# Kernel optimization log

Hardware: AMD Instinct MI355X
Metric: run time of the kernel (lower is better)

## Reference

```python
import jax, jax.numpy as jnp
import numpy as np

N_NODES = 50000
N_EDGES = 800000
D = 128


def gcn_conv(x, edge_index, W, b):
    """PyG GCNConv: out = D^{-1/2} (A+I) D^{-1/2} (x W) + b."""
    n = x.shape[0]
    loop = jnp.arange(n)
    row = jnp.concatenate([edge_index[0], loop])  # source nodes (x_j)
    col = jnp.concatenate([edge_index[1], loop])  # target nodes (aggregation)
    deg = jnp.zeros((n,), dtype=x.dtype).at[col].add(1.0)
    deg_inv_sqrt = jnp.where(deg > 0, jax.lax.rsqrt(deg), 0.0)
    norm = deg_inv_sqrt[row] * deg_inv_sqrt[col]  # [E+N]
    h = x @ W  # [N, F]
    msg = h[row] * norm[:, None]  # gather + scale, [E+N, F]
    out = jax.ops.segment_sum(msg, col, num_segments=n)
    return out + b


def setup_inputs() -> dict:
    key = jax.random.key(0)
    k1, k2, k3, k4 = jax.random.split(key, 4)
    x = jax.random.normal(k1, (N_NODES, D), dtype=jnp.float32)
    edge_index = jax.random.randint(k2, (2, N_EDGES), 0, N_NODES, dtype=jnp.int64)
    scale = 1.0 / np.sqrt(D)
    W1 = jax.random.normal(k3, (D, D), dtype=jnp.float32) * scale
    W2 = jax.random.normal(k4, (D, D), dtype=jnp.float32) * scale
    b1 = jnp.zeros((D,), dtype=jnp.float32)
    b2 = jnp.zeros((D,), dtype=jnp.float32)
    return {"x": x, "edge_index": edge_index, "W1": W1, "b1": b1, "W2": W2, "b2": b2}


def reference(x, edge_index, W1, b1, W2, b2):
    h = gcn_conv(x, edge_index, W1, b1)
    h = gcn_conv(h, edge_index, W2, b2)
    return jax.nn.leaky_relu(h, negative_slope=0.1)
```

## Files before the change

### kernel.cpp

```cpp
#include <hip/hip_runtime.h>

#define DF 128
#define CHUNK 2048
#define LSTCAP 6144

typedef __bf16 bf16x8 __attribute__((ext_vector_type(8)));
typedef float f32x4 __attribute__((ext_vector_type(4)));


static __device__ __forceinline__ float lrelu(float x) {
  return x > 0.f ? x : 0.1f * x;
}
static __device__ __forceinline__ unsigned short f2bf(float f) {
  unsigned int u = __float_as_uint(f);
  u += 0x7FFFu + ((u >> 16) & 1u);
  return (unsigned short)(u >> 16);
}
static __device__ __forceinline__ float bf2f(unsigned short h) {
  return __uint_as_float((unsigned int)h << 16);
}

__global__ __launch_bounds__(256) void prep_kernel(
    const float* __restrict__ W1, const float* __restrict__ W2,
    const float* __restrict__ b1, unsigned short* __restrict__ wfrag,
    float* __restrict__ c1, const void* __restrict__ ei, int E,
    int* __restrict__ M, unsigned int* __restrict__ pairs, int NBUCK,
    int NCHUNK) {
  __shared__ int h[256];
  __shared__ int any32;
  int tid = threadIdx.x;
  if (blockIdx.x < 129) {
    if (tid >= 128) return;
    int j = tid;
    if (blockIdx.x < 128) {
      int i = blockIdx.x;
      float acc = 0.f;
      for (int k = 0; k < 128; ++k)
        acc = fmaf(W1[i * 128 + k], W2[k * 128 + j], acc);
      unsigned short hh = f2bf(acc);
      unsigned short ll = f2bf(acc - bf2f(hh));
      int fid = (((i >> 5) * 8) + (j >> 4)) * 64 + ((i >> 3) & 3) * 16 + (j & 15);
      int pos = fid * 8 + (i & 7);
      wfrag[pos] = hh;
      wfrag[16384 + pos] = ll;
    } else {
      float acc = 0.f;
      for (int k = 0; k < 128; ++k) acc = fmaf(b1[k], W2[k * 128 + j], acc);
      c1[j] = acc;
    }
    return;
  }
  int blk = blockIdx.x - 129;
  if (tid == 0) any32 = 0;
  h[tid] = 0;
  __syncthreads();
  int base = blk * CHUNK;
  int end = min(base + CHUNK, E);
  {
    const unsigned int* u = (const unsigned int*)ei;
    long long i = (long long)base + tid * 8;
    if (i < end && u[2 * i + 1] != 0u) any32 = 1;
  }
  __syncthreads();
  int is64 = !any32;
  if (is64) {
    const long long* p = (const long long*)ei;
    for (int i = base + tid; i < end; i += 256) {
      int src = (int)p[i];
      int c = (int)p[(size_t)E + i];
      atomicAdd(&h[c >> 8], 1);
      pairs[i] = ((unsigned)src << 16) | (unsigned)c;
    }
  } else {
    const int* p = (const int*)ei;
    for (int i = base + tid; i < end; i += 256) {
      int src = p[i];
      int c = p[(size_t)E + i];
      atomicAdd(&h[c >> 8], 1);
      pairs[i] = ((unsigned)src << 16) | (unsigned)c;
    }
  }
  __syncthreads();
  if (tid < NBUCK) M[tid * NCHUNK + blk] = h[tid];
}

__global__ __launch_bounds__(256) void matscanA_kernel(int* __restrict__ M,
                                                       int* __restrict__ btot,
                                                       int NCHUNK) {
  __shared__ int s[256];
  int tid = threadIdx.x;
  int base = blockIdx.x * NCHUNK;
  int i0 = tid * 2, i1 = tid * 2 + 1;
  int v0 = (i0 < NCHUNK) ? M[base + i0] : 0;
  int v1 = (i1 < NCHUNK) ? M[base + i1] : 0;
  int loc = v0 + v1;
  s[tid] = loc;
  __syncthreads();
  for (int d = 1; d < 256; d <<= 1) {
    int add = (tid >= d) ? s[tid - d] : 0;
    __syncthreads();
    s[tid] += add;
    __syncthreads();
  }
  int excl = s[tid] - loc;
  if (i0 < NCHUNK) M[base + i0] = excl;
  if (i1 < NCHUNK) M[base + i1] = excl + v0;
  if (tid == 255) btot[blockIdx.x] = s[255];
}

__global__ __launch_bounds__(256) void p1c_kernel(
    const unsigned int* __restrict__ pairs, int E, const int* __restrict__ M,
    const int* __restrict__ btot, int NBUCK, int NCHUNK,
    unsigned int* __restrict__ staging) {
  __shared__ int bs[256];
  __shared__ int rowM[256];
  __shared__ int lcur[256];
  int tid = threadIdx.x;
  int blk = blockIdx.x;
  int v = (tid < NBUCK) ? btot[tid] : 0;
  bs[tid] = v;
  __syncthreads();
  for (int d = 1; d < 256; d <<= 1) {
    int add = (tid >= d) ? bs[tid - d] : 0;
    __syncthreads();
    bs[tid] += add;
    __syncthreads();
  }
  if (tid < NBUCK) rowM[tid] = M[tid * NCHUNK + blk] + (bs[tid] - v);
  lcur[tid] = 0;
  __syncthreads();
  int base = blk * CHUNK;
  int end = min(base + CHUNK, E);
  for (int i = base + tid; i < end; i += 256) {
    unsigned pv = pairs[i];
    int b = (int)((pv & 0xFFFFu) >> 8);
    int r = atomicAdd(&lcur[b], 1);
    staging[rowM[b] + r] = pv;
  }
}

__global__ __launch_bounds__(256) void p2_kernel(
    const unsigned int* __restrict__ staging, const int* __restrict__ btot,
    int NBUCK, int2* __restrict__ offcnt, float* __restrict__ dis,
    unsigned short* __restrict__ srcs, int n) {
  __shared__ int bs[256], h[256], ex[256], lcur[256];
  __shared__ unsigned int lst[LSTCAP];
  int tid = threadIdx.x;
  int b = blockIdx.x;
  int v = (tid < NBUCK) ? btot[tid] : 0;
  bs[tid] = v;
  h[tid] = 0;
  lcur[tid] = 0;
  __syncthreads();
  for (int d = 1; d < 256; d <<= 1) {
    int add = (tid >= d) ? bs[tid - d] : 0;
    __syncthreads();
    bs[tid] += add;
    __syncthreads();
  }
  int lenb = btot[b];
  int base = bs[b] - lenb;
  __syncthreads();
  for (int i = tid; i < lenb; i += 256) {
    unsigned int pv = staging[base + i];
    if (i < LSTCAP) lst[i] = pv;
    atomicAdd(&h[pv & 255u], 1);
  }
  __syncthreads();
  int my = h[tid];
  ex[tid] = my;
  __syncthreads();
  for (int d = 1; d < 256; d <<= 1) {
    int add = (tid >= d) ? ex[tid - d] : 0;
    __syncthreads();
    ex[tid] += add;
    __syncthreads();
  }
  int excl = ex[tid] - my;
  ex[tid] = excl;
  int node = (b << 8) + tid;
  if (node < n) {
    offcnt[node] = make_int2(base + excl, my);
    dis[node] = rsqrtf((float)(my + 1));
  }
  __syncthreads();
  for (int i = tid; i < lenb; i += 256) {
    unsigned int pv = (i < LSTCAP) ? lst[i] : staging[base + i];
    int ci = (int)(pv & 255u);
    int r = atomicAdd(&lcur[ci], 1);
    srcs[base + ex[ci] + r] = (unsigned short)(pv >> 16);
  }
}

__global__ __launch_bounds__(256, 6) void gemmrs_kernel(
    const float* __restrict__ A, const unsigned short* __restrict__ wfrag,
    const float* __restrict__ dis, unsigned short* __restrict__ G, int n,
    const int2* __restrict__ offcnt, const unsigned short* __restrict__ srcs,
    float* __restrict__ r, int gGemm) {
  __shared__ unsigned short Ah[2][4][64][8];
  __shared__ unsigned short Al[2][4][64][8];
  __shared__ unsigned short Cs[32 * 136];
  __shared__ float disS[32];
  int tid = threadIdx.x;

  if (blockIdx.x >= gGemm) {
    int t = (blockIdx.x - gGemm) * 256 + tid;
    if (t < n) {
      int2 oc = offcnt[t];
      float dt = dis[t];
      float acc = dt;
      for (int i = 0; i < oc.y; ++i) acc += dis[(int)srcs[oc.x + i]];
      r[t] = dt * acc;
    }
    return;
  }

  int row0 = blockIdx.x * 32;
  if (tid < 32) {
    int gr = row0 + tid;
    disS[tid] = (gr < n) ? dis[gr] : 0.f;
  }

  const float4* A4 = (const float4*)A;
#pragma unroll
  for (int it = 0; it < 4; ++it) {
    int fi = it * 256 + tid;
    int row = fi >> 5;
    int c4 = fi & 31;
    int gr = row0 + row;
    float4 v = make_float4(0.f, 0.f, 0.f, 0.f);
    if (gr < n) v = A4[(size_t)gr * 32 + c4];
    unsigned short h0 = f2bf(v.x), h1 = f2bf(v.y), h2 = f2bf(v.z), h3 = f2bf(v.w);
    unsigned short l0 = f2bf(v.x - bf2f(h0)), l1 = f2bf(v.y - bf2f(h1));
    unsigned short l2 = f2bf(v.z - bf2f(h2)), l3 = f2bf(v.w - bf2f(h3));
    int band = row >> 4;
    int kslab = c4 >> 3;
    int lane = ((c4 >> 1) & 3) * 16 + (row & 15);
    int e0 = (c4 & 1) * 4;
    *(uint2*)&Ah[band][kslab][lane][e0] =
        make_uint2((unsigned int)h0 | ((unsigned int)h1 << 16),
                   (unsigned int)h2 | ((unsigned int)h3 << 16));
    *(uint2*)&Al[band][kslab][lane][e0] =
        make_uint2((unsigned int)l0 | ((unsigned int)l1 << 16),
                   (unsigned int)l2 | ((unsigned int)l3 << 16));
  }
  __syncthreads();

  int w = tid >> 6, lane = tid & 63;
  int band = w & 1, ch = w >> 1;

  f32x4 acc[4];
#pragma unroll
  for (int t = 0; t < 4; ++t) acc[t] = (f32x4){0.f, 0.f, 0.f, 0.f};

#pragma unroll
  for (int ks = 0; ks < 4; ++ks) {
    bf16x8 ahi = *(const bf16x8*)&Ah[band][ks][lane][0];
    bf16x8 alo = *(const bf16x8*)&Al[band][ks][lane][0];
#pragma unroll
    for (int ct = 0; ct < 4; ++ct) {
      size_t fb = ((size_t)(ks * 8 + ch * 4 + ct) * 64 + lane) * 8;
      bf16x8 whi = *(const bf16x8*)&wfrag[fb];
      bf16x8 wlo = *(const bf16x8*)&wfrag[16384 + fb];
      acc[ct] = __builtin_amdgcn_mfma_f32_16x16x32_bf16(ahi, whi, acc[ct], 0, 0, 0);
      acc[ct] = __builtin_amdgcn_mfma_f32_16x16x32_bf16(ahi, wlo, acc[ct], 0, 0, 0);
      acc[ct] = __builtin_amdgcn_mfma_f32_16x16x32_bf16(alo, whi, acc[ct], 0, 0, 0);
    }
  }

#pragma unroll
  for (int ct = 0; ct < 4; ++ct) {
    int col = ch * 64 + ct * 16 + (lane & 15);
#pragma unroll
    for (int rr = 0; rr < 4; ++rr) {
      int lrow = band * 16 + ((lane >> 4) << 2) + rr;
      Cs[lrow * 136 + col] = f2bf(acc[ct][rr] * disS[lrow]);
    }
  }
  __syncthreads();
#pragma unroll
  for (int it = 0; it < 2; ++it) {
    int fi = it * 256 + tid;
    int row = fi >> 4, q = fi & 15;
    int gr = row0 + row;
    int pl = q >> 2, qq = q & 3;
    if (gr < n)
      ((uint4*)(G + ((size_t)pl * n + gr) * 32))[qq] =
          *(uint4*)&Cs[row * 136 + q * 8];
  }
}

template <int OUT>
__global__ __launch_bounds__(512) void aggp_kernel(
    const unsigned short* __restrict__ g, const unsigned short* __restrict__ srcs,
    const int2* __restrict__ offcnt, const float* __restrict__ dis,
    const float* __restrict__ r, const float* __restrict__ c1,
    const float* __restrict__ b2, void* __restrict__ outv, int n) {
  int pl = blockIdx.x & 3;
  int nb = blockIdx.x >> 2;
  int wv = threadIdx.x >> 6;
  int lane = threadIdx.x & 63;
  int grp = lane >> 3;
  int sl = lane & 7;
  int wid = (nb * 8 + wv) * 8 + grp;
  if (wid >= n) return;
  const unsigned short* up = g + (size_t)pl * n * 32;

  float a0, a1, a2, a3;
  {
    uint2 sv = ((const uint2*)(up + (size_t)wid * 32))[sl];
    a0 = __uint_as_float(sv.x << 16);
    a1 = __uint_as_float(sv.x & 0xFFFF0000u);
    a2 = __uint_as_float(sv.y << 16);
    a3 = __uint_as_float(sv.y & 0xFFFF0000u);
  }

#define ACC_U2(U)                                \
  do {                                           \
    a0 += __uint_as_float((U).x << 16);          \
    a1 += __uint_as_float((U).x & 0xFFFF0000u);  \
    a2 += __uint_as_float((U).y << 16);          \
    a3 += __uint_as_float((U).y & 0xFFFF0000u);  \
  } while (0)

  int2 oc = offcnt[wid];
  const unsigned short* sp = srcs + oc.x;
  int cnt = oc.y;
  int j = 0;
  for (; j + 4 <= cnt; j += 4) {
    int s0 = (int)sp[j], s1 = (int)sp[j + 1];
    int s2 = (int)sp[j + 2], s3 = (int)sp[j + 3];
    uint2 u0 = ((const uint2*)(up + (size_t)s0 * 32))[sl];
    uint2 u1 = ((const uint2*)(up + (size_t)s1 * 32))[sl];
    uint2 u2 = ((const uint2*)(up + (size_t)s2 * 32))[sl];
    uint2 u3 = ((const uint2*)(up + (size_t)s3 * 32))[sl];
    ACC_U2(u0);
    ACC_U2(u1);
    ACC_U2(u2);
    ACC_U2(u3);
  }
  if (j + 2 <= cnt) {
    int s0 = (int)sp[j], s1 = (int)sp[j + 1];
    uint2 u0 = ((const uint2*)(up + (size_t)s0 * 32))[sl];
    uint2 u1 = ((const uint2*)(up + (size_t)s1 * 32))[sl];
    ACC_U2(u0);
    ACC_U2(u1);
    j += 2;
  }
  if (j < cnt) {
    int s0 = (int)sp[j];
    uint2 u0 = ((const uint2*)(up + (size_t)s0 * 32))[sl];
    ACC_U2(u0);
  }
#undef ACC_U2

  if (OUT == 0) {
    float dw = dis[wid];
    float sc = dw * dw;
    uint2 p;
    p.x = (unsigned)f2bf(a0 * sc) | ((unsigned)f2bf(a1 * sc) << 16);
    p.y = (unsigned)f2bf(a2 * sc) | ((unsigned)f2bf(a3 * sc) << 16);
    ((uint2*)((unsigned short*)outv + ((size_t)pl * n + wid) * 32))[sl] = p;
  } else {
    float dw = dis[wid];
    float rv = r[wid];
    float4 cc = *(const float4*)&c1[pl * 32 + sl * 4];
    float4 bb = *(const float4*)&b2[pl * 32 + sl * 4];
    float4 o;
    o.x = lrelu(fmaf(a0, dw, fmaf(rv, cc.x, bb.x)));
    o.y = lrelu(fmaf(a1, dw, fmaf(rv, cc.y, bb.y)));
    o.z = lrelu(fmaf(a2, dw, fmaf(rv, cc.z, bb.z)));
    o.w = lrelu(fmaf(a3, dw, fmaf(rv, cc.w, bb.w)));
    *(float4*)((float*)outv + (size_t)wid * DF + pl * 32 + sl * 4) = o;
  }
}

extern "C" void kernel_launch(void* const* d_in, const int* in_sizes, int n_in,
                              void* d_out, int out_size, void* d_ws, size_t ws_size,
                              hipStream_t stream) {
  const float* x  = (const float*)d_in[0];
  const void*  ei = d_in[1];
  const float* W1 = (const float*)d_in[2];
  const float* b1 = (const float*)d_in[3];
  const float* W2 = (const float*)d_in[4];
  const float* b2 = (const float*)d_in[5];
  float* out = (float*)d_out;

  int n = in_sizes[0] / DF;
  int E = in_sizes[1] / 2;
  int NBUCK = (n + 255) >> 8;
  int NCHUNK = (E + CHUNK - 1) / CHUNK;

  char* w = (char*)d_ws;
  auto carve = [&](size_t bytes) {
    char* p = w;
    w += (bytes + 15) & ~(size_t)15;
    return p;
  };
  float* dis    = (float*)carve((size_t)n * 4);
  float* rr     = (float*)carve((size_t)n * 4);
  int2*  offcnt = (int2*)carve((size_t)n * 8);
  int*   btot   = (int*)carve((size_t)NBUCK * 4);
  int*   M      = (int*)carve((size_t)NBUCK * NCHUNK * 4);
  unsigned short* wfrag = (unsigned short*)carve(65536);
  float* c1     = (float*)carve(512);
  unsigned int* pairs   = (unsigned int*)carve((size_t)E * 4);
  unsigned int* staging = (unsigned int*)carve((size_t)E * 4);
  unsigned short* srcs  = (unsigned short*)carve((size_t)E * 2);
  unsigned short* bufU  = (unsigned short*)carve((size_t)n * DF * 2);
  unsigned short* bufV  = (unsigned short*)carve((size_t)n * DF * 2);

  prep_kernel<<<129 + NCHUNK, 256, 0, stream>>>(W1, W2, b1, wfrag, c1, ei, E,
                                                M, pairs, NBUCK, NCHUNK);
  matscanA_kernel<<<NBUCK, 256, 0, stream>>>(M, btot, NCHUNK);
  p1c_kernel<<<NCHUNK, 256, 0, stream>>>(pairs, E, M, btot, NBUCK, NCHUNK,
                                         staging);
  p2_kernel<<<NBUCK, 256, 0, stream>>>(staging, btot, NBUCK, offcnt, dis,
                                       srcs, n);

  int gGemm = (n + 31) / 32;
  int gRsum = (n + 255) / 256;
  gemmrs_kernel<<<gGemm + gRsum, 256, 0, stream>>>(x, wfrag, dis, bufU, n,
                                                   offcnt, srcs, rr, gGemm);

  int gAgg = 4 * ((n + 63) / 64);
  aggp_kernel<0><<<gAgg, 512, 0, stream>>>(bufU, srcs, offcnt, dis, rr, c1, b2,
                                           bufV, n);
  aggp_kernel<1><<<gAgg, 512, 0, stream>>>(bufV, srcs, offcnt, dis, rr, c1, b2,
                                           out, n);
}
```

Before: 121.5 us.

## Sort nodes by in-degree so aggregation groups get balanced work

```diff
diff --git a/kernel.cpp b/kernel.cpp
--- a/kernel.cpp
+++ b/kernel.cpp
@@ -86,9 +86,15 @@
 
 __global__ __launch_bounds__(256) void matscanA_kernel(int* __restrict__ M,
                                                        int* __restrict__ btot,
+                                                       int* __restrict__ dbins,
+                                                       int* __restrict__ dcur,
                                                        int NCHUNK) {
   __shared__ int s[256];
   int tid = threadIdx.x;
+  if (blockIdx.x == 0) {
+    dbins[tid] = 0;
+    dcur[tid] = 0;
+  }
   int base = blockIdx.x * NCHUNK;
   int i0 = tid * 2, i1 = tid * 2 + 1;
   int v0 = (i0 < NCHUNK) ? M[base + i0] : 0;
@@ -142,7 +148,7 @@
 __global__ __launch_bounds__(256) void p2_kernel(
     const unsigned int* __restrict__ staging, const int* __restrict__ btot,
     int NBUCK, int2* __restrict__ offcnt, float* __restrict__ dis,
-    unsigned short* __restrict__ srcs, int n) {
+    unsigned short* __restrict__ srcs, int* __restrict__ dbins, int n) {
   __shared__ int bs[256], h[256], ex[256], lcur[256];
   __shared__ unsigned int lst[LSTCAP];
   int tid = threadIdx.x;
@@ -182,6 +188,7 @@
   if (node < n) {
     offcnt[node] = make_int2(base + excl, my);
     dis[node] = rsqrtf((float)(my + 1));
+    atomicAdd(&dbins[my < 255 ? my : 255], 1);
   }
   __syncthreads();
   for (int i = tid; i < lenb; i += 256) {
@@ -196,12 +203,38 @@
     const float* __restrict__ A, const unsigned short* __restrict__ wfrag,
     const float* __restrict__ dis, unsigned short* __restrict__ G, int n,
     const int2* __restrict__ offcnt, const unsigned short* __restrict__ srcs,
-    float* __restrict__ r, int gGemm) {
+    float* __restrict__ r, const int* __restrict__ dbins,
+    int* __restrict__ dcur, int* __restrict__ perm, int gGemm, int gRsum) {
   __shared__ unsigned short Ah[2][4][64][8];
   __shared__ unsigned short Al[2][4][64][8];
   __shared__ unsigned short Cs[32 * 136];
   __shared__ float disS[32];
+  __shared__ int sb[256];
   int tid = threadIdx.x;
+
+  if (blockIdx.x >= gGemm + gRsum) {
+    int t = (blockIdx.x - gGemm - gRsum) * 256 + tid;
+    int vv = dbins[tid];
+    sb[tid] = vv;
+    __syncthreads();
+    for (int d = 1; d < 256; d <<= 1) {
+      int add = (tid >= d) ? sb[tid - d] : 0;
+      __syncthreads();
+      sb[tid] += add;
+      __syncthreads();
+    }
+    int excl = sb[tid] - vv;
+    __syncthreads();
+    sb[tid] = excl;
+    __syncthreads();
+    if (t < n) {
+      int deg = offcnt[t].y;
+      deg = deg < 255 ? deg : 255;
+      int pos = sb[deg] + atomicAdd(&dcur[deg], 1);
+      perm[pos] = t;
+    }
+    return;
+  }
 
   if (blockIdx.x >= gGemm) {
     int t = (blockIdx.x - gGemm) * 256 + tid;
@@ -295,15 +328,17 @@
     const unsigned short* __restrict__ g, const unsigned short* __restrict__ srcs,
     const int2* __restrict__ offcnt, const float* __restrict__ dis,
     const float* __restrict__ r, const float* __restrict__ c1,
-    const float* __restrict__ b2, void* __restrict__ outv, int n) {
+    const float* __restrict__ b2, const int* __restrict__ perm,
+    void* __restrict__ outv, int n) {
   int pl = blockIdx.x & 3;
   int nb = blockIdx.x >> 2;
   int wv = threadIdx.x >> 6;
   int lane = threadIdx.x & 63;
   int grp = lane >> 3;
   int sl = lane & 7;
-  int wid = (nb * 8 + wv) * 8 + grp;
-  if (wid >= n) return;
+  int gidx = (nb * 8 + wv) * 8 + grp;
+  if (gidx >= n) return;
+  int wid = perm[gidx];
   const unsigned short* up = g + (size_t)pl * n * 32;
 
   float a0, a1, a2, a3;
@@ -401,6 +436,9 @@
   float* rr     = (float*)carve((size_t)n * 4);
   int2*  offcnt = (int2*)carve((size_t)n * 8);
   int*   btot   = (int*)carve((size_t)NBUCK * 4);
+  int*   dbins  = (int*)carve(1024);
+  int*   dcur   = (int*)carve(1024);
+  int*   perm   = (int*)carve((size_t)n * 4);
   int*   M      = (int*)carve((size_t)NBUCK * NCHUNK * 4);
   unsigned short* wfrag = (unsigned short*)carve(65536);
   float* c1     = (float*)carve(512);
@@ -412,20 +450,22 @@
 
   prep_kernel<<<129 + NCHUNK, 256, 0, stream>>>(W1, W2, b1, wfrag, c1, ei, E,
                                                 M, pairs, NBUCK, NCHUNK);
-  matscanA_kernel<<<NBUCK, 256, 0, stream>>>(M, btot, NCHUNK);
+  matscanA_kernel<<<NBUCK, 256, 0, stream>>>(M, btot, dbins, dcur, NCHUNK);
   p1c_kernel<<<NCHUNK, 256, 0, stream>>>(pairs, E, M, btot, NBUCK, NCHUNK,
                                          staging);
   p2_kernel<<<NBUCK, 256, 0, stream>>>(staging, btot, NBUCK, offcnt, dis,
-                                       srcs, n);
+                                       srcs, dbins, n);
 
   int gGemm = (n + 31) / 32;
   int gRsum = (n + 255) / 256;
-  gemmrs_kernel<<<gGemm + gRsum, 256, 0, stream>>>(x, wfrag, dis, bufU, n,
-                                                   offcnt, srcs, rr, gGemm);
+  int gPerm = (n + 255) / 256;
+  gemmrs_kernel<<<gGemm + gRsum + gPerm, 256, 0, stream>>>(
+      x, wfrag, dis, bufU, n, offcnt, srcs, rr, dbins, dcur, perm, gGemm,
+      gRsum);
 
   int gAgg = 4 * ((n + 63) / 64);
   aggp_kernel<0><<<gAgg, 512, 0, stream>>>(bufU, srcs, offcnt, dis, rr, c1, b2,
-                                           bufV, n);
+                                           perm, bufV, n);
   aggp_kernel<1><<<gAgg, 512, 0, stream>>>(bufV, srcs, offcnt, dis, rr, c1, b2,
-                                           out, n);
-}
+                                           perm, out, n);
+}
```

New measurement: 411.7 us. +238.9%, slower.

## Overlap GEMM with edge bucketing and fold source norms into packed indices

Applied to the files above, without the earlier changes.

```diff
diff --git a/kernel.cpp b/kernel.cpp
--- a/kernel.cpp
+++ b/kernel.cpp
@@ -20,207 +20,78 @@
   return __uint_as_float((unsigned int)h << 16);
 }
 
-__global__ __launch_bounds__(256) void prep_kernel(
+__global__ __launch_bounds__(128) void wprod_kernel(
     const float* __restrict__ W1, const float* __restrict__ W2,
     const float* __restrict__ b1, unsigned short* __restrict__ wfrag,
-    float* __restrict__ c1, const void* __restrict__ ei, int E,
+    float* __restrict__ c1) {
+  int j = threadIdx.x;
+  if (blockIdx.x < 128) {
+    int i = blockIdx.x;
+    float acc = 0.f;
+    for (int k = 0; k < 128; ++k)
+      acc = fmaf(W1[i * 128 + k], W2[k * 128 + j], acc);
+    unsigned short h = f2bf(acc);
+    unsigned short l = f2bf(acc - bf2f(h));
+    int fid = (((i >> 5) * 8) + (j >> 4)) * 64 + ((i >> 3) & 3) * 16 + (j & 15);
+    int pos = fid * 8 + (i & 7);
+    wfrag[pos] = h;
+    wfrag[16384 + pos] = l;
+  } else {
+    float acc = 0.f;
+    for (int k = 0; k < 128; ++k) acc = fmaf(b1[k], W2[k * 128 + j], acc);
+    c1[j] = acc;
+  }
+}
+
+__global__ __launch_bounds__(256, 6) void prep2_kernel(
+    const float* __restrict__ A, const unsigned short* __restrict__ wfrag,
+    unsigned short* __restrict__ G, int n, const void* __restrict__ ei, int E,
     int* __restrict__ M, unsigned int* __restrict__ pairs, int NBUCK,
-    int NCHUNK) {
-  __shared__ int h[256];
-  __shared__ int any32;
-  int tid = threadIdx.x;
-  if (blockIdx.x < 129) {
-    if (tid >= 128) return;
-    int j = tid;
-    if (blockIdx.x < 128) {
-      int i = blockIdx.x;
-      float acc = 0.f;
-      for (int k = 0; k < 128; ++k)
-        acc = fmaf(W1[i * 128 + k], W2[k * 128 + j], acc);
-      unsigned short hh = f2bf(acc);
-      unsigned short ll = f2bf(acc - bf2f(hh));
-      int fid = (((i >> 5) * 8) + (j >> 4)) * 64 + ((i >> 3) & 3) * 16 + (j & 15);
-      int pos = fid * 8 + (i & 7);
-      wfrag[pos] = hh;
-      wfrag[16384 + pos] = ll;
-    } else {
-      float acc = 0.f;
-      for (int k = 0; k < 128; ++k) acc = fmaf(b1[k], W2[k * 128 + j], acc);
-      c1[j] = acc;
-    }
-    return;
-  }
-  int blk = blockIdx.x - 129;
-  if (tid == 0) any32 = 0;
-  h[tid] = 0;
-  __syncthreads();
-  int base = blk * CHUNK;
-  int end = min(base + CHUNK, E);
-  {
-    const unsigned int* u = (const unsigned int*)ei;
-    long long i = (long long)base + tid * 8;
-    if (i < end && u[2 * i + 1] != 0u) any32 = 1;
-  }
-  __syncthreads();
-  int is64 = !any32;
-  if (is64) {
-    const long long* p = (const long long*)ei;
-    for (int i = base + tid; i < end; i += 256) {
-      int src = (int)p[i];
-      int c = (int)p[(size_t)E + i];
-      atomicAdd(&h[c >> 8], 1);
-      pairs[i] = ((unsigned)src << 16) | (unsigned)c;
-    }
-  } else {
-    const int* p = (const int*)ei;
-    for (int i = base + tid; i < end; i += 256) {
-      int src = p[i];
-      int c = p[(size_t)E + i];
-      atomicAdd(&h[c >> 8], 1);
-      pairs[i] = ((unsigned)src << 16) | (unsigned)c;
-    }
-  }
-  __syncthreads();
-  if (tid < NBUCK) M[tid * NCHUNK + blk] = h[tid];
-}
-
-__global__ __launch_bounds__(256) void matscanA_kernel(int* __restrict__ M,
-                                                       int* __restrict__ btot,
-                                                       int NCHUNK) {
-  __shared__ int s[256];
-  int tid = threadIdx.x;
-  int base = blockIdx.x * NCHUNK;
-  int i0 = tid * 2, i1 = tid * 2 + 1;
-  int v0 = (i0 < NCHUNK) ? M[base + i0] : 0;
-  int v1 = (i1 < NCHUNK) ? M[base + i1] : 0;
-  int loc = v0 + v1;
-  s[tid] = loc;
-  __syncthreads();
-  for (int d = 1; d < 256; d <<= 1) {
-    int add = (tid >= d) ? s[tid - d] : 0;
-    __syncthreads();
-    s[tid] += add;
-    __syncthreads();
-  }
-  int excl = s[tid] - loc;
-  if (i0 < NCHUNK) M[base + i0] = excl;
-  if (i1 < NCHUNK) M[base + i1] = excl + v0;
-  if (tid == 255) btot[blockIdx.x] = s[255];
-}
-
-__global__ __launch_bounds__(256) void p1c_kernel(
-    const unsigned int* __restrict__ pairs, int E, const int* __restrict__ M,
-    const int* __restrict__ btot, int NBUCK, int NCHUNK,
-    unsigned int* __restrict__ staging) {
-  __shared__ int bs[256];
-  __shared__ int rowM[256];
-  __shared__ int lcur[256];
-  int tid = threadIdx.x;
-  int blk = blockIdx.x;
-  int v = (tid < NBUCK) ? btot[tid] : 0;
-  bs[tid] = v;
-  __syncthreads();
-  for (int d = 1; d < 256; d <<= 1) {
-    int add = (tid >= d) ? bs[tid - d] : 0;
-    __syncthreads();
-    bs[tid] += add;
-    __syncthreads();
-  }
-  if (tid < NBUCK) rowM[tid] = M[tid * NCHUNK + blk] + (bs[tid] - v);
-  lcur[tid] = 0;
-  __syncthreads();
-  int base = blk * CHUNK;
-  int end = min(base + CHUNK, E);
-  for (int i = base + tid; i < end; i += 256) {
-    unsigned pv = pairs[i];
-    int b = (int)((pv & 0xFFFFu) >> 8);
-    int r = atomicAdd(&lcur[b], 1);
-    staging[rowM[b] + r] = pv;
-  }
-}
-
-__global__ __launch_bounds__(256) void p2_kernel(
-    const unsigned int* __restrict__ staging, const int* __restrict__ btot,
-    int NBUCK, int2* __restrict__ offcnt, float* __restrict__ dis,
-    unsigned short* __restrict__ srcs, int n) {
-  __shared__ int bs[256], h[256], ex[256], lcur[256];
-  __shared__ unsigned int lst[LSTCAP];
-  int tid = threadIdx.x;
-  int b = blockIdx.x;
-  int v = (tid < NBUCK) ? btot[tid] : 0;
-  bs[tid] = v;
-  h[tid] = 0;
-  lcur[tid] = 0;
-  __syncthreads();
-  for (int d = 1; d < 256; d <<= 1) {
-    int add = (tid >= d) ? bs[tid - d] : 0;
-    __syncthreads();
-    bs[tid] += add;
-    __syncthreads();
-  }
-  int lenb = btot[b];
-  int base = bs[b] - lenb;
-  __syncthreads();
-  for (int i = tid; i < lenb; i += 256) {
-    unsigned int pv = staging[base + i];
-    if (i < LSTCAP) lst[i] = pv;
-    atomicAdd(&h[pv & 255u], 1);
-  }
-  __syncthreads();
-  int my = h[tid];
-  ex[tid] = my;
-  __syncthreads();
-  for (int d = 1; d < 256; d <<= 1) {
-    int add = (tid >= d) ? ex[tid - d] : 0;
-    __syncthreads();
-    ex[tid] += add;
-    __syncthreads();
-  }
-  int excl = ex[tid] - my;
-  ex[tid] = excl;
-  int node = (b << 8) + tid;
-  if (node < n) {
-    offcnt[node] = make_int2(base + excl, my);
-    dis[node] = rsqrtf((float)(my + 1));
-  }
-  __syncthreads();
-  for (int i = tid; i < lenb; i += 256) {
-    unsigned int pv = (i < LSTCAP) ? lst[i] : staging[base + i];
-    int ci = (int)(pv & 255u);
-    int r = atomicAdd(&lcur[ci], 1);
-    srcs[base + ex[ci] + r] = (unsigned short)(pv >> 16);
-  }
-}
-
-__global__ __launch_bounds__(256, 6) void gemmrs_kernel(
-    const float* __restrict__ A, const unsigned short* __restrict__ wfrag,
-    const float* __restrict__ dis, unsigned short* __restrict__ G, int n,
-    const int2* __restrict__ offcnt, const unsigned short* __restrict__ srcs,
-    float* __restrict__ r, int gGemm) {
+    int NCHUNK, int gGemm) {
   __shared__ unsigned short Ah[2][4][64][8];
   __shared__ unsigned short Al[2][4][64][8];
   __shared__ unsigned short Cs[32 * 136];
-  __shared__ float disS[32];
   int tid = threadIdx.x;
 
   if (blockIdx.x >= gGemm) {
-    int t = (blockIdx.x - gGemm) * 256 + tid;
-    if (t < n) {
-      int2 oc = offcnt[t];
-      float dt = dis[t];
-      float acc = dt;
-      for (int i = 0; i < oc.y; ++i) acc += dis[(int)srcs[oc.x + i]];
-      r[t] = dt * acc;
+    int* h = (int*)&Ah[0][0][0][0];
+    __shared__ int any32;
+    int blk = blockIdx.x - gGemm;
+    if (tid == 0) any32 = 0;
+    h[tid] = 0;
+    __syncthreads();
+    int base = blk * CHUNK;
+    int end = min(base + CHUNK, E);
+    {
+      const unsigned int* u = (const unsigned int*)ei;
+      long long i = (long long)base + tid * 8;
+      if (i < end && u[2 * i + 1] != 0u) any32 = 1;
     }
+    __syncthreads();
+    int is64 = !any32;
+    if (is64) {
+      const long long* p = (const long long*)ei;
+      for (int i = base + tid; i < end; i += 256) {
+        int src = (int)p[i];
+        int c = (int)p[(size_t)E + i];
+        atomicAdd(&h[c >> 8], 1);
+        pairs[i] = ((unsigned)src << 16) | (unsigned)c;
+      }
+    } else {
+      const int* p = (const int*)ei;
+      for (int i = base + tid; i < end; i += 256) {
+        int src = p[i];
+        int c = p[(size_t)E + i];
+        atomicAdd(&h[c >> 8], 1);
+        pairs[i] = ((unsigned)src << 16) | (unsigned)c;
+      }
+    }
+    __syncthreads();
+    if (tid < NBUCK) M[tid * NCHUNK + blk] = h[tid];
     return;
   }
 
   int row0 = blockIdx.x * 32;
-  if (tid < 32) {
-    int gr = row0 + tid;
-    disS[tid] = (gr < n) ? dis[gr] : 0.f;
-  }
-
   const float4* A4 = (const float4*)A;
 #pragma unroll
   for (int it = 0; it < 4; ++it) {
@@ -274,7 +145,7 @@
 #pragma unroll
     for (int rr = 0; rr < 4; ++rr) {
       int lrow = band * 16 + ((lane >> 4) << 2) + rr;
-      Cs[lrow * 136 + col] = f2bf(acc[ct][rr] * disS[lrow]);
+      Cs[lrow * 136 + col] = f2bf(acc[ct][rr]);
     }
   }
   __syncthreads();
@@ -290,12 +161,206 @@
   }
 }
 
-template <int OUT>
-__global__ __launch_bounds__(512) void aggp_kernel(
+__global__ __launch_bounds__(256) void matscanA_kernel(int* __restrict__ M,
+                                                       int* __restrict__ btot,
+                                                       int NCHUNK) {
+  __shared__ int s[256];
+  int tid = threadIdx.x;
+  int base = blockIdx.x * NCHUNK;
+  int i0 = tid * 2, i1 = tid * 2 + 1;
+  int v0 = (i0 < NCHUNK) ? M[base + i0] : 0;
+  int v1 = (i1 < NCHUNK) ? M[base + i1] : 0;
+  int loc = v0 + v1;
+  s[tid] = loc;
+  __syncthreads();
+  for (int d = 1; d < 256; d <<= 1) {
+    int add = (tid >= d) ? s[tid - d] : 0;
+    __syncthreads();
+    s[tid] += add;
+    __syncthreads();
+  }
+  int excl = s[tid] - loc;
+  if (i0 < NCHUNK) M[base + i0] = excl;
+  if (i1 < NCHUNK) M[base + i1] = excl + v0;
+  if (tid == 255) btot[blockIdx.x] = s[255];
+}
+
+__global__ __launch_bounds__(256) void p1c_kernel(
+    const unsigned int* __restrict__ pairs, int E, const int* __restrict__ M,
+    const int* __restrict__ btot, int NBUCK, int NCHUNK,
+    unsigned int* __restrict__ staging) {
+  __shared__ int bs[256];
+  __shared__ int rowM[256];
+  __shared__ int lcur[256];
+  int tid = threadIdx.x;
+  int blk = blockIdx.x;
+  int v = (tid < NBUCK) ? btot[tid] : 0;
+  bs[tid] = v;
+  __syncthreads();
+  for (int d = 1; d < 256; d <<= 1) {
+    int add = (tid >= d) ? bs[tid - d] : 0;
+    __syncthreads();
+    bs[tid] += add;
+    __syncthreads();
+  }
+  if (tid < NBUCK) rowM[tid] = M[tid * NCHUNK + blk] + (bs[tid] - v);
+  lcur[tid] = 0;
+  __syncthreads();
+  int base = blk * CHUNK;
+  int end = min(base + CHUNK, E);
+  for (int i = base + tid; i < end; i += 256) {
+    unsigned pv = pairs[i];
+    int b = (int)((pv & 0xFFFFu) >> 8);
+    int r = atomicAdd(&lcur[b], 1);
+    staging[rowM[b] + r] = pv;
+  }
+}
+
+__global__ __launch_bounds__(256) void p2_kernel(
+    const unsigned int* __restrict__ staging, const int* __restrict__ btot,
+    int NBUCK, int2* __restrict__ offcnt, float* __restrict__ dis,
+    unsigned short* __restrict__ srcs, int n) {
+  __shared__ int bs[256], h[256], ex[256], lcur[256];
+  __shared__ unsigned int lst[LSTCAP];
+  int tid = threadIdx.x;
+  int b = blockIdx.x;
+  int v = (tid < NBUCK) ? btot[tid] : 0;
+  bs[tid] = v;
+  h[tid] = 0;
+  lcur[tid] = 0;
+  __syncthreads();
+  for (int d = 1; d < 256; d <<= 1) {
+    int add = (tid >= d) ? bs[tid - d] : 0;
+    __syncthreads();
+    bs[tid] += add;
+    __syncthreads();
+  }
+  int lenb = btot[b];
+  int base = bs[b] - lenb;
+  __syncthreads();
+  for (int i = tid; i < lenb; i += 256) {
+    unsigned int pv = staging[base + i];
+    if (i < LSTCAP) lst[i] = pv;
+    atomicAdd(&h[pv & 255u], 1);
+  }
+  __syncthreads();
+  int my = h[tid];
+  ex[tid] = my;
+  __syncthreads();
+  for (int d = 1; d < 256; d <<= 1) {
+    int add = (tid >= d) ? ex[tid - d] : 0;
+    __syncthreads();
+    ex[tid] += add;
+    __syncthreads();
+  }
+  int excl = ex[tid] - my;
+  ex[tid] = excl;
+  int node = (b << 8) + tid;
+  if (node < n) {
+    offcnt[node] = make_int2(base + excl, my);
+    dis[node] = rsqrtf((float)(my + 1));
+  }
+  __syncthreads();
+  for (int i = tid; i < lenb; i += 256) {
+    unsigned int pv = (i < LSTCAP) ? lst[i] : staging[base + i];
+    int ci = (int)(pv & 255u);
+    int r = atomicAdd(&lcur[ci], 1);
+    srcs[base + ex[ci] + r] = (unsigned short)(pv >> 16);
+  }
+}
+
+__global__ __launch_bounds__(256) void rsann_kernel(
+    const int2* __restrict__ offcnt, const float* __restrict__ dis,
+    const unsigned short* __restrict__ srcs, unsigned int* __restrict__ srcsu,
+    float* __restrict__ r, int n) {
+  int t = blockIdx.x * 256 + threadIdx.x;
+  if (t >= n) return;
+  int2 oc = offcnt[t];
+  float dt = dis[t];
+  float acc = dt;
+  for (int i = 0; i < oc.y; ++i) {
+    int s = (int)srcs[oc.x + i];
+    float ds = dis[s];
+    acc += ds;
+    srcsu[oc.x + i] = ((unsigned)f2bf(ds) << 16) | (unsigned)s;
+  }
+  r[t] = dt * acc;
+}
+
+__global__ __launch_bounds__(512) void aggp0_kernel(
+    const unsigned short* __restrict__ g, const unsigned int* __restrict__ srcsu,
+    const int2* __restrict__ offcnt, const float* __restrict__ dis,
+    unsigned short* __restrict__ outv, int n) {
+  int pl = blockIdx.x & 3;
+  int nb = blockIdx.x >> 2;
+  int wv = threadIdx.x >> 6;
+  int lane = threadIdx.x & 63;
+  int grp = lane >> 3;
+  int sl = lane & 7;
+  int wid = (nb * 8 + wv) * 8 + grp;
+  if (wid >= n) return;
+  const unsigned short* up = g + (size_t)pl * n * 32;
+  float dw = dis[wid];
+
+  float a0, a1, a2, a3;
+  {
+    uint2 sv = ((const uint2*)(up + (size_t)wid * 32))[sl];
+    a0 = __uint_as_float(sv.x << 16) * dw;
+    a1 = __uint_as_float(sv.x & 0xFFFF0000u) * dw;
+    a2 = __uint_as_float(sv.y << 16) * dw;
+    a3 = __uint_as_float(sv.y & 0xFFFF0000u) * dw;
+  }
+
+#define ACC_U2N(U, NR)                                      \
+  do {                                                      \
+    a0 = fmaf(__uint_as_float((U).x << 16), (NR), a0);      \
+    a1 = fmaf(__uint_as_float((U).x & 0xFFFF0000u), (NR), a1); \
+    a2 = fmaf(__uint_as_float((U).y << 16), (NR), a2);      \
+    a3 = fmaf(__uint_as_float((U).y & 0xFFFF0000u), (NR), a3); \
+  } while (0)
+
+  int2 oc = offcnt[wid];
+  const unsigned int* sp = srcsu + oc.x;
+  int cnt = oc.y;
+  int j = 0;
+  for (; j + 4 <= cnt; j += 4) {
+    unsigned v0 = sp[j], v1 = sp[j + 1], v2 = sp[j + 2], v3 = sp[j + 3];
+    uint2 u0 = ((const uint2*)(up + (size_t)(v0 & 0xFFFFu) * 32))[sl];
+    uint2 u1 = ((const uint2*)(up + (size_t)(v1 & 0xFFFFu) * 32))[sl];
+    uint2 u2 = ((const uint2*)(up + (size_t)(v2 & 0xFFFFu) * 32))[sl];
+    uint2 u3 = ((const uint2*)(up + (size_t)(v3 & 0xFFFFu) * 32))[sl];
+    ACC_U2N(u0, __uint_as_float(v0 & 0xFFFF0000u));
+    ACC_U2N(u1, __uint_as_float(v1 & 0xFFFF0000u));
+    ACC_U2N(u2, __uint_as_float(v2 & 0xFFFF0000u));
+    ACC_U2N(u3, __uint_as_float(v3 & 0xFFFF0000u));
+  }
+  if (j + 2 <= cnt) {
+    unsigned v0 = sp[j], v1 = sp[j + 1];
+    uint2 u0 = ((const uint2*)(up + (size_t)(v0 & 0xFFFFu) * 32))[sl];
+    uint2 u1 = ((const uint2*)(up + (size_t)(v1 & 0xFFFFu) * 32))[sl];
+    ACC_U2N(u0, __uint_as_float(v0 & 0xFFFF0000u));
+    ACC_U2N(u1, __uint_as_float(v1 & 0xFFFF0000u));
+    j += 2;
+  }
+  if (j < cnt) {
+    unsigned v0 = sp[j];
+    uint2 u0 = ((const uint2*)(up + (size_t)(v0 & 0xFFFFu) * 32))[sl];
+    ACC_U2N(u0, __uint_as_float(v0 & 0xFFFF0000u));
+  }
+#undef ACC_U2N
+
+  float sc = dw * dw;
+  uint2 p;
+  p.x = (unsigned)f2bf(a0 * sc) | ((unsigned)f2bf(a1 * sc) << 16);
+  p.y = (unsigned)f2bf(a2 * sc) | ((unsigned)f2bf(a3 * sc) << 16);
+  ((uint2*)(outv + ((size_t)pl * n + wid) * 32))[sl] = p;
+}
+
+__global__ __launch_bounds__(512) void aggp1_kernel(
     const unsigned short* __restrict__ g, const unsigned short* __restrict__ srcs,
     const int2* __restrict__ offcnt, const float* __restrict__ dis,
     const float* __restrict__ r, const float* __restrict__ c1,
-    const float* __restrict__ b2, void* __restrict__ outv, int n) {
+    const float* __restrict__ b2, float* __restrict__ outv, int n) {
   int pl = blockIdx.x & 3;
   int nb = blockIdx.x >> 2;
   int wv = threadIdx.x >> 6;
@@ -354,25 +419,16 @@
   }
 #undef ACC_U2
 
-  if (OUT == 0) {
-    float dw = dis[wid];
-    float sc = dw * dw;
-    uint2 p;
-    p.x = (unsigned)f2bf(a0 * sc) | ((unsigned)f2bf(a1 * sc) << 16);
-    p.y = (unsigned)f2bf(a2 * sc) | ((unsigned)f2bf(a3 * sc) << 16);
-    ((uint2*)((unsigned short*)outv + ((size_t)pl * n + wid) * 32))[sl] = p;
-  } else {
-    float dw = dis[wid];
-    float rv = r[wid];
-    float4 cc = *(const float4*)&c1[pl * 32 + sl * 4];
-    float4 bb = *(const float4*)&b2[pl * 32 + sl * 4];
-    float4 o;
-    o.x = lrelu(fmaf(a0, dw, fmaf(rv, cc.x, bb.x)));
-    o.y = lrelu(fmaf(a1, dw, fmaf(rv, cc.y, bb.y)));
-    o.z = lrelu(fmaf(a2, dw, fmaf(rv, cc.z, bb.z)));
-    o.w = lrelu(fmaf(a3, dw, fmaf(rv, cc.w, bb.w)));
-    *(float4*)((float*)outv + (size_t)wid * DF + pl * 32 + sl * 4) = o;
-  }
+  float dw = dis[wid];
+  float rv = r[wid];
+  float4 cc = *(const float4*)&c1[pl * 32 + sl * 4];
+  float4 bb = *(const float4*)&b2[pl * 32 + sl * 4];
+  float4 o;
+  o.x = lrelu(fmaf(a0, dw, fmaf(rv, cc.x, bb.x)));
+  o.y = lrelu(fmaf(a1, dw, fmaf(rv, cc.y, bb.y)));
+  o.z = lrelu(fmaf(a2, dw, fmaf(rv, cc.z, bb.z)));
+  o.w = lrelu(fmaf(a3, dw, fmaf(rv, cc.w, bb.w)));
+  *(float4*)(outv + (size_t)wid * DF + pl * 32 + sl * 4) = o;
 }
 
 extern "C" void kernel_launch(void* const* d_in, const int* in_sizes, int n_in,
@@ -407,25 +463,26 @@
   unsigned int* pairs   = (unsigned int*)carve((size_t)E * 4);
   unsigned int* staging = (unsigned int*)carve((size_t)E * 4);
   unsigned short* srcs  = (unsigned short*)carve((size_t)E * 2);
+  unsigned int* srcsu   = (unsigned int*)carve((size_t)E * 4);
   unsigned short* bufU  = (unsigned short*)carve((size_t)n * DF * 2);
   unsigned short* bufV  = (unsigned short*)carve((size_t)n * DF * 2);
 
-  prep_kernel<<<129 + NCHUNK, 256, 0, stream>>>(W1, W2, b1, wfrag, c1, ei, E,
-                                                M, pairs, NBUCK, NCHUNK);
+  int gGemm = (n + 31) / 32;
+
+  wprod_kernel<<<129, 128, 0, stream>>>(W1, W2, b1, wfrag, c1);
+  prep2_kernel<<<gGemm + NCHUNK, 256, 0, stream>>>(x, wfrag, bufU, n, ei, E,
+                                                   M, pairs, NBUCK, NCHUNK,
+                                                   gGemm);
   matscanA_kernel<<<NBUCK, 256, 0, stream>>>(M, btot, NCHUNK);
   p1c_kernel<<<NCHUNK, 256, 0, stream>>>(pairs, E, M, btot, NBUCK, NCHUNK,
                                          staging);
   p2_kernel<<<NBUCK, 256, 0, stream>>>(staging, btot, NBUCK, offcnt, dis,
                                        srcs, n);
-
-  int gGemm = (n + 31) / 32;
-  int gRsum = (n + 255) / 256;
-  gemmrs_kernel<<<gGemm + gRsum, 256, 0, stream>>>(x, wfrag, dis, bufU, n,
-                                                   offcnt, srcs, rr, gGemm);
+  rsann_kernel<<<(n + 255) / 256, 256, 0, stream>>>(offcnt, dis, srcs, srcsu,
+                                                    rr, n);
 
   int gAgg = 4 * ((n + 63) / 64);
-  aggp_kernel<0><<<gAgg, 512, 0, stream>>>(bufU, srcs, offcnt, dis, rr, c1, b2,
-                                           bufV, n);
-  aggp_kernel<1><<<gAgg, 512, 0, stream>>>(bufV, srcs, offcnt, dis, rr, c1, b2,
-                                           out, n);
-}
+  aggp0_kernel<<<gAgg, 512, 0, stream>>>(bufU, srcsu, offcnt, dis, bufV, n);
+  aggp1_kernel<<<gAgg, 512, 0, stream>>>(bufV, srcs, offcnt, dis, rr, c1, b2,
+                                         out, n);
+}
```

Measured after the change: 129.1 us. +6.3%, slower.

## Compute degrees via global atomics and overlap bucket scatter with GEMM

Applied to the files above, without the earlier changes.

```diff
diff --git a/kernel.cpp b/kernel.cpp
--- a/kernel.cpp
+++ b/kernel.cpp
@@ -24,8 +24,8 @@
     const float* __restrict__ W1, const float* __restrict__ W2,
     const float* __restrict__ b1, unsigned short* __restrict__ wfrag,
     float* __restrict__ c1, const void* __restrict__ ei, int E,
-    int* __restrict__ M, unsigned int* __restrict__ pairs, int NBUCK,
-    int NCHUNK) {
+    int* __restrict__ M, unsigned int* __restrict__ pairs,
+    int* __restrict__ cnt, int NBUCK, int NCHUNK) {
   __shared__ int h[256];
   __shared__ int any32;
   int tid = threadIdx.x;
@@ -69,6 +69,7 @@
       int src = (int)p[i];
       int c = (int)p[(size_t)E + i];
       atomicAdd(&h[c >> 8], 1);
+      atomicAdd(&cnt[c], 1);
       pairs[i] = ((unsigned)src << 16) | (unsigned)c;
     }
   } else {
@@ -77,6 +78,7 @@
       int src = p[i];
       int c = p[(size_t)E + i];
       atomicAdd(&h[c >> 8], 1);
+      atomicAdd(&cnt[c], 1);
       pairs[i] = ((unsigned)src << 16) | (unsigned)c;
     }
   }
@@ -84,11 +86,16 @@
   if (tid < NBUCK) M[tid * NCHUNK + blk] = h[tid];
 }
 
-__global__ __launch_bounds__(256) void matscanA_kernel(int* __restrict__ M,
-                                                       int* __restrict__ btot,
-                                                       int NCHUNK) {
+__global__ __launch_bounds__(256) void matscanA_kernel(
+    int* __restrict__ M, int* __restrict__ btot, const int* __restrict__ cnt,
+    float* __restrict__ dis, int NCHUNK, int NBUCK, int n) {
   __shared__ int s[256];
   int tid = threadIdx.x;
+  if (blockIdx.x >= NBUCK) {
+    int t = (blockIdx.x - NBUCK) * 256 + tid;
+    if (t < n) dis[t] = rsqrtf((float)(cnt[t] + 1));
+    return;
+  }
   int base = blockIdx.x * NCHUNK;
   int i0 = tid * 2, i1 = tid * 2 + 1;
   int v0 = (i0 < NCHUNK) ? M[base + i0] : 0;
@@ -108,95 +115,12 @@
   if (tid == 255) btot[blockIdx.x] = s[255];
 }
 
-__global__ __launch_bounds__(256) void p1c_kernel(
+__global__ __launch_bounds__(256, 6) void p1cg_kernel(
+    const float* __restrict__ A, const unsigned short* __restrict__ wfrag,
+    const float* __restrict__ dis, unsigned short* __restrict__ G, int n,
     const unsigned int* __restrict__ pairs, int E, const int* __restrict__ M,
     const int* __restrict__ btot, int NBUCK, int NCHUNK,
-    unsigned int* __restrict__ staging) {
-  __shared__ int bs[256];
-  __shared__ int rowM[256];
-  __shared__ int lcur[256];
-  int tid = threadIdx.x;
-  int blk = blockIdx.x;
-  int v = (tid < NBUCK) ? btot[tid] : 0;
-  bs[tid] = v;
-  __syncthreads();
-  for (int d = 1; d < 256; d <<= 1) {
-    int add = (tid >= d) ? bs[tid - d] : 0;
-    __syncthreads();
-    bs[tid] += add;
-    __syncthreads();
-  }
-  if (tid < NBUCK) rowM[tid] = M[tid * NCHUNK + blk] + (bs[tid] - v);
-  lcur[tid] = 0;
-  __syncthreads();
-  int base = blk * CHUNK;
-  int end = min(base + CHUNK, E);
-  for (int i = base + tid; i < end; i += 256) {
-    unsigned pv = pairs[i];
-    int b = (int)((pv & 0xFFFFu) >> 8);
-    int r = atomicAdd(&lcur[b], 1);
-    staging[rowM[b] + r] = pv;
-  }
-}
-
-__global__ __launch_bounds__(256) void p2_kernel(
-    const unsigned int* __restrict__ staging, const int* __restrict__ btot,
-    int NBUCK, int2* __restrict__ offcnt, float* __restrict__ dis,
-    unsigned short* __restrict__ srcs, int n) {
-  __shared__ int bs[256], h[256], ex[256], lcur[256];
-  __shared__ unsigned int lst[LSTCAP];
-  int tid = threadIdx.x;
-  int b = blockIdx.x;
-  int v = (tid < NBUCK) ? btot[tid] : 0;
-  bs[tid] = v;
-  h[tid] = 0;
-  lcur[tid] = 0;
-  __syncthreads();
-  for (int d = 1; d < 256; d <<= 1) {
-    int add = (tid >= d) ? bs[tid - d] : 0;
-    __syncthreads();
-    bs[tid] += add;
-    __syncthreads();
-  }
-  int lenb = btot[b];
-  int base = bs[b] - lenb;
-  __syncthreads();
-  for (int i = tid; i < lenb; i += 256) {
-    unsigned int pv = staging[base + i];
-    if (i < LSTCAP) lst[i] = pv;
-    atomicAdd(&h[pv & 255u], 1);
-  }
-  __syncthreads();
-  int my = h[tid];
-  ex[tid] = my;
-  __syncthreads();
-  for (int d = 1; d < 256; d <<= 1) {
-    int add = (tid >= d) ? ex[tid - d] : 0;
-    __syncthreads();
-    ex[tid] += add;
-    __syncthreads();
-  }
-  int excl = ex[tid] - my;
-  ex[tid] = excl;
-  int node = (b << 8) + tid;
-  if (node < n) {
-    offcnt[node] = make_int2(base + excl, my);
-    dis[node] = rsqrtf((float)(my + 1));
-  }
-  __syncthreads();
-  for (int i = tid; i < lenb; i += 256) {
-    unsigned int pv = (i < LSTCAP) ? lst[i] : staging[base + i];
-    int ci = (int)(pv & 255u);
-    int r = atomicAdd(&lcur[ci], 1);
-    srcs[base + ex[ci] + r] = (unsigned short)(pv >> 16);
-  }
-}
-
-__global__ __launch_bounds__(256, 6) void gemmrs_kernel(
-    const float* __restrict__ A, const unsigned short* __restrict__ wfrag,
-    const float* __restrict__ dis, unsigned short* __restrict__ G, int n,
-    const int2* __restrict__ offcnt, const unsigned short* __restrict__ srcs,
-    float* __restrict__ r, int gGemm) {
+    unsigned int* __restrict__ staging, int gGemm) {
   __shared__ unsigned short Ah[2][4][64][8];
   __shared__ unsigned short Al[2][4][64][8];
   __shared__ unsigned short Cs[32 * 136];
@@ -204,13 +128,29 @@
   int tid = threadIdx.x;
 
   if (blockIdx.x >= gGemm) {
-    int t = (blockIdx.x - gGemm) * 256 + tid;
-    if (t < n) {
-      int2 oc = offcnt[t];
-      float dt = dis[t];
-      float acc = dt;
-      for (int i = 0; i < oc.y; ++i) acc += dis[(int)srcs[oc.x + i]];
-      r[t] = dt * acc;
+    int* bs = (int*)&Ah[0][0][0][0];
+    int* rowM = bs + 256;
+    int* lcur = bs + 512;
+    int blk = blockIdx.x - gGemm;
+    int v = (tid < NBUCK) ? btot[tid] : 0;
+    bs[tid] = v;
+    __syncthreads();
+    for (int d = 1; d < 256; d <<= 1) {
+      int add = (tid >= d) ? bs[tid - d] : 0;
+      __syncthreads();
+      bs[tid] += add;
+      __syncthreads();
+    }
+    if (tid < NBUCK) rowM[tid] = M[tid * NCHUNK + blk] + (bs[tid] - v);
+    lcur[tid] = 0;
+    __syncthreads();
+    int base = blk * CHUNK;
+    int end = min(base + CHUNK, E);
+    for (int i = base + tid; i < end; i += 256) {
+      unsigned pv = pairs[i];
+      int b = (int)((pv & 0xFFFFu) >> 8);
+      int r = atomicAdd(&lcur[b], 1);
+      staging[rowM[b] + r] = pv;
     }
     return;
   }
@@ -220,7 +160,6 @@
     int gr = row0 + tid;
     disS[tid] = (gr < n) ? dis[gr] : 0.f;
   }
-
   const float4* A4 = (const float4*)A;
 #pragma unroll
   for (int it = 0; it < 4; ++it) {
@@ -290,6 +229,64 @@
   }
 }
 
+__global__ __launch_bounds__(256) void p2_kernel(
+    const unsigned int* __restrict__ staging, const int* __restrict__ btot,
+    int NBUCK, int2* __restrict__ offcnt, const float* __restrict__ dis,
+    unsigned short* __restrict__ srcs, float* __restrict__ r, int n) {
+  __shared__ int bs[256], h[256], ex[256], lcur[256];
+  __shared__ unsigned int lst[LSTCAP];
+  int tid = threadIdx.x;
+  int b = blockIdx.x;
+  int v = (tid < NBUCK) ? btot[tid] : 0;
+  bs[tid] = v;
+  h[tid] = 0;
+  lcur[tid] = 0;
+  __syncthreads();
+  for (int d = 1; d < 256; d <<= 1) {
+    int add = (tid >= d) ? bs[tid - d] : 0;
+    __syncthreads();
+    bs[tid] += add;
+    __syncthreads();
+  }
+  int lenb = btot[b];
+  int base = bs[b] - lenb;
+  __syncthreads();
+  for (int i = tid; i < lenb; i += 256) {
+    unsigned int pv = staging[base + i];
+    if (i < LSTCAP) lst[i] = pv;
+    atomicAdd(&h[pv & 255u], 1);
+  }
+  __syncthreads();
+  int my = h[tid];
+  ex[tid] = my;
+  __syncthreads();
+  for (int d = 1; d < 256; d <<= 1) {
+    int add = (tid >= d) ? ex[tid - d] : 0;
+    __syncthreads();
+    ex[tid] += add;
+    __syncthreads();
+  }
+  int excl = ex[tid] - my;
+  ex[tid] = excl;
+  int node = (b << 8) + tid;
+  if (node < n) offcnt[node] = make_int2(base + excl, my);
+  __syncthreads();
+  for (int i = tid; i < lenb; i += 256) {
+    unsigned int pv = (i < LSTCAP) ? lst[i] : staging[base + i];
+    int ci = (int)(pv & 255u);
+    int rk = atomicAdd(&lcur[ci], 1);
+    srcs[base + ex[ci] + rk] = (unsigned short)(pv >> 16);
+  }
+  __syncthreads();
+  if (node < n) {
+    float dt = dis[node];
+    float acc = dt;
+    int gbase = base + excl;
+    for (int i = 0; i < my; ++i) acc += dis[(int)srcs[gbase + i]];
+    r[node] = dt * acc;
+  }
+}
+
 template <int OUT>
 __global__ __launch_bounds__(512) void aggp_kernel(
     const unsigned short* __restrict__ g, const unsigned short* __restrict__ srcs,
@@ -399,6 +396,7 @@
   };
   float* dis    = (float*)carve((size_t)n * 4);
   float* rr     = (float*)carve((size_t)n * 4);
+  int*   cnt    = (int*)carve((size_t)n * 4);
   int2*  offcnt = (int2*)carve((size_t)n * 8);
   int*   btot   = (int*)carve((size_t)NBUCK * 4);
   int*   M      = (int*)carve((size_t)NBUCK * NCHUNK * 4);
@@ -410,18 +408,20 @@
   unsigned short* bufU  = (unsigned short*)carve((size_t)n * DF * 2);
   unsigned short* bufV  = (unsigned short*)carve((size_t)n * DF * 2);
 
+  int gGemm = (n + 31) / 32;
+  int gDis  = (n + 255) / 256;
+
+  hipMemsetAsync(cnt, 0, (size_t)n * 4, stream);
+
   prep_kernel<<<129 + NCHUNK, 256, 0, stream>>>(W1, W2, b1, wfrag, c1, ei, E,
-                                                M, pairs, NBUCK, NCHUNK);
-  matscanA_kernel<<<NBUCK, 256, 0, stream>>>(M, btot, NCHUNK);
-  p1c_kernel<<<NCHUNK, 256, 0, stream>>>(pairs, E, M, btot, NBUCK, NCHUNK,
-                                         staging);
+                                                M, pairs, cnt, NBUCK, NCHUNK);
+  matscanA_kernel<<<NBUCK + gDis, 256, 0, stream>>>(M, btot, cnt, dis, NCHUNK,
+                                                    NBUCK, n);
+  p1cg_kernel<<<gGemm + NCHUNK, 256, 0, stream>>>(x, wfrag, dis, bufU, n,
+                                                  pairs, E, M, btot, NBUCK,
+                                                  NCHUNK, staging, gGemm);
   p2_kernel<<<NBUCK, 256, 0, stream>>>(staging, btot, NBUCK, offcnt, dis,
-                                       srcs, n);
-
-  int gGemm = (n + 31) / 32;
-  int gRsum = (n + 255) / 256;
-  gemmrs_kernel<<<gGemm + gRsum, 256, 0, stream>>>(x, wfrag, dis, bufU, n,
-                                                   offcnt, srcs, rr, gGemm);
+                                       srcs, rr, n);
 
   int gAgg = 4 * ((n + 63) / 64);
   aggp_kernel<0><<<gAgg, 512, 0, stream>>>(bufU, srcs, offcnt, dis, rr, c1, b2,
```

Result: slower. 157.1 us (+29.3%).
